# Performance work log

Hardware: AMD Instinct MI355X
Metric: run time of the kernel (lower is better)

The kernel has to match this reference:

```python
import jax, jax.numpy as jnp
import numpy as np

B, M, N = 16384, 512, 2048
N_ITERS = 10


def setup_inputs() -> dict:
    key = jax.random.key(0)
    kb, kD = jax.random.split(key)
    batch = jax.random.normal(kb, (B, M), dtype=jnp.float32)
    # nn.Parameter(torch.rand((M, N))) -> uniform [0,1)
    D = jax.random.uniform(kD, (M, N), dtype=jnp.float32)
    gamma = jnp.float32(0.1)
    beta = jnp.float32(0.1)
    return {"batch": batch, "D": D, "gamma": gamma, "beta": beta}


def reference(batch, D, gamma, beta):
    # Vectorized AMP sparse coding: the original loops over batch items; here
    # the per-sample matvecs D.T@v and D@alpha become batched GEMMs v@D, a@D.T.
    y = batch                                   # [B, M]
    m = D.shape[0]
    sqrt_m = jnp.sqrt(jnp.asarray(m, y.dtype))
    alpha0 = jnp.zeros((y.shape[0], D.shape[1]), dtype=y.dtype)  # [B, N]

    def amp_step(carry, _):
        alpha, v = carry
        z = alpha + beta * (v @ D)                               # [B, N]
        # per-sample threshold t = gamma/sqrt(M) * ||v||_2
        t = (gamma / sqrt_m) * jnp.linalg.norm(v, axis=-1, keepdims=True)  # [B,1]
        new_alpha = jnp.maximum(z - t, 0.0) * jnp.sign(z)        # relu(z-t)*sign(z)
        new_v = (y - beta * (new_alpha @ D.T)
                 + (beta / m) * jnp.linalg.norm(new_alpha, axis=-1, keepdims=True) * v)
        return (new_alpha, new_v), None

    (alpha, _v), _ = jax.lax.scan(amp_step, (alpha0, y), None, length=N_ITERS)
    return alpha
```

## Files before the change

kernel.cpp:

```cpp
#include <hip/hip_runtime.h>
#include <math.h>

#define Bsz 16384
#define Msz 512
#define Nsz 2048

typedef _Float16 half8 __attribute__((ext_vector_type(8)));
typedef _Float16 half4 __attribute__((ext_vector_type(4)));
typedef _Float16 half2v __attribute__((ext_vector_type(2)));
typedef float floatx16 __attribute__((ext_vector_type(16)));
typedef unsigned int uint;

__device__ __forceinline__ void gl_lds16(const _Float16* g, _Float16* l) {
    __builtin_amdgcn_global_load_lds(
        (const __attribute__((address_space(1))) unsigned int*)g,
        (__attribute__((address_space(3))) unsigned int*)l, 16, 0, 0);
}

#define BAR()  asm volatile("s_barrier" ::: "memory")


__global__ __launch_bounds__(256) void zero_kernel(float4* __restrict__ p) {
    p[blockIdx.x * 256 + threadIdx.x] = make_float4(0.f, 0.f, 0.f, 0.f);
}

__global__ __launch_bounds__(256) void init_kernel(const float* __restrict__ batch,
        _Float16* __restrict__ vh, float* __restrict__ t2) {
    const int wave = threadIdx.x >> 6;
    const int lane = threadIdx.x & 63;
    const int b = (blockIdx.x << 2) + wave;
    const float* row = batch + (size_t)b * Msz + lane * 8;
    float4 a = *(const float4*)row;
    float4 c = *(const float4*)(row + 4);
    half8 h;
    h[0] = (_Float16)a.x; h[1] = (_Float16)a.y;
    h[2] = (_Float16)a.z; h[3] = (_Float16)a.w;
    h[4] = (_Float16)c.x; h[5] = (_Float16)c.y;
    h[6] = (_Float16)c.z; h[7] = (_Float16)c.w;
    const size_t off = ((size_t)(b >> 5) * 32 + (lane >> 1)) * 512
                     + ((size_t)(lane & 1) << 8) + ((b & 31) << 3);
    *(half8*)(vh + off) = h;
    float s = a.x*a.x + a.y*a.y + a.z*a.z + a.w*a.w
            + c.x*c.x + c.y*c.y + c.z*c.z + c.w*c.w;
#pragma unroll
    for (int off2 = 32; off2 > 0; off2 >>= 1) s += __shfl_down(s, off2);
    if (lane == 0) t2[b] = s;
}

__global__ __launch_bounds__(256) void convD_kernel(const float* __restrict__ D,
        _Float16* __restrict__ Dph, _Float16* __restrict__ Dtph) {
    __shared__ float T[64][65];
    const int t = threadIdx.x;
    const int tx = t & 15, ty = t >> 4;
    const int n0 = blockIdx.x << 6, m0 = blockIdx.y << 6;
#pragma unroll
    for (int q = 0; q < 4; ++q) {
        const int mr = m0 + (ty << 2) + q;
        const int nc = n0 + (tx << 2);
        float4 d = *(const float4*)(D + (size_t)mr * Nsz + nc);
        half4 h;
        h[0] = (_Float16)d.x; h[1] = (_Float16)d.y;
        h[2] = (_Float16)d.z; h[3] = (_Float16)d.w;
        const size_t o2 = ((size_t)(mr >> 5) * 128 + (nc >> 4)) * 512
                        + (((size_t)(nc >> 3) & 1) << 8) + ((mr & 31) << 3) + (nc & 7);
        *(half4*)(Dph + o2) = h;
        T[(tx << 2) + 0][(ty << 2) + q] = d.x;
        T[(tx << 2) + 1][(ty << 2) + q] = d.y;
        T[(tx << 2) + 2][(ty << 2) + q] = d.z;
        T[(tx << 2) + 3][(ty << 2) + q] = d.w;
    }
    __syncthreads();
#pragma unroll
    for (int q = 0; q < 4; ++q) {
        const int nr = n0 + (ty << 2) + q;
        const int mc = m0 + (tx << 2);
        float4 d = make_float4(T[(ty << 2) + q][tx << 2],
                               T[(ty << 2) + q][(tx << 2) + 1],
                               T[(ty << 2) + q][(tx << 2) + 2],
                               T[(ty << 2) + q][(tx << 2) + 3]);
        half4 h;
        h[0] = (_Float16)d.x; h[1] = (_Float16)d.y;
        h[2] = (_Float16)d.z; h[3] = (_Float16)d.w;
        const size_t o1 = ((size_t)(nr >> 5) * 32 + (mc >> 4)) * 512
                        + (((size_t)(mc >> 3) & 1) << 8) + ((nr & 31) << 3) + (mc & 7);
        *(half4*)(Dtph + o1) = h;
    }
}

template<int FIRST, int LAST>
__global__ __launch_bounds__(256, 4) void gemm1_kernel(
        const _Float16* __restrict__ Av,
        const _Float16* __restrict__ Bth,
        const float* __restrict__ t2,
        _Float16* __restrict__ alphaH,
        float* __restrict__ out,
        float* __restrict__ na2,
        const float* __restrict__ beta_p, const float* __restrict__ gamma_p) {
    const int tid = threadIdx.x;
    const int wave = tid >> 6, lane = tid & 63;
    const int wy = wave >> 1, wx = wave & 1;
    const int ln = lane & 31, lh = lane >> 5;
    const int bid = blockIdx.x;
    const int b0 = (bid & 127) << 7;
    const int n0 = (bid >> 7) << 7;
    const int R0 = b0 >> 5, C0 = n0 >> 5;

    floatx16 acc[2][2] = {};

    const _Float16* pa0 = Av  + ((size_t)(R0 + 2 * wy)     * 32) * 512 + lane * 8;
    const _Float16* pa1 = Av  + ((size_t)(R0 + 2 * wy + 1) * 32) * 512 + lane * 8;
    const _Float16* pb0 = Bth + ((size_t)(C0 + 2 * wx)     * 32) * 512 + lane * 8;
    const _Float16* pb1 = Bth + ((size_t)(C0 + 2 * wx + 1) * 32) * 512 + lane * 8;

    half8 xa0, xa1, xb0, xb1;
    half8 ya0, ya1, yb0, yb1;

    xa0 = *(const half8*)(pa0);
    xa1 = *(const half8*)(pa1);
    xb0 = *(const half8*)(pb0);
    xb1 = *(const half8*)(pb1);

    for (int kt = 0; kt < 32; kt += 2) {
        {
            const size_t o = (size_t)(kt + 1) << 9;
            ya0 = *(const half8*)(pa0 + o);
            ya1 = *(const half8*)(pa1 + o);
            yb0 = *(const half8*)(pb0 + o);
            yb1 = *(const half8*)(pb1 + o);
            acc[0][0] = __builtin_amdgcn_mfma_f32_32x32x16_f16(xa0, xb0, acc[0][0], 0, 0, 0);
            acc[1][0] = __builtin_amdgcn_mfma_f32_32x32x16_f16(xa1, xb0, acc[1][0], 0, 0, 0);
            acc[0][1] = __builtin_amdgcn_mfma_f32_32x32x16_f16(xa0, xb1, acc[0][1], 0, 0, 0);
            acc[1][1] = __builtin_amdgcn_mfma_f32_32x32x16_f16(xa1, xb1, acc[1][1], 0, 0, 0);
        }
        {
            if (kt + 2 < 32) {
                const size_t o = (size_t)(kt + 2) << 9;
                xa0 = *(const half8*)(pa0 + o);
                xa1 = *(const half8*)(pa1 + o);
                xb0 = *(const half8*)(pb0 + o);
                xb1 = *(const half8*)(pb1 + o);
            }
            acc[0][0] = __builtin_amdgcn_mfma_f32_32x32x16_f16(ya0, yb0, acc[0][0], 0, 0, 0);
            acc[1][0] = __builtin_amdgcn_mfma_f32_32x32x16_f16(ya1, yb0, acc[1][0], 0, 0, 0);
            acc[0][1] = __builtin_amdgcn_mfma_f32_32x32x16_f16(ya0, yb1, acc[0][1], 0, 0, 0);
            acc[1][1] = __builtin_amdgcn_mfma_f32_32x32x16_f16(ya1, yb1, acc[1][1], 0, 0, 0);
        }
    }

    const float beta = beta_p[0];
    const float tc = gamma_p[0] * 0.044194173824159216f;
#pragma unroll
    for (int i = 0; i < 2; ++i) {
#pragma unroll
        for (int reg = 0; reg < 16; ++reg) {
            const int rr = (reg & 3) + 8 * (reg >> 2) + 4 * lh;
            const int b = b0 + wy * 64 + i * 32 + rr;
            const float tb2 = tc * sqrtf(t2[b]);
            const size_t rbase = (size_t)b * Nsz + n0 + wx * 64 + ln;
            _Float16* arow = alphaH + rbase;
            float s = 0.f;
#pragma unroll
            for (int j = 0; j < 2; ++j) {
                float z = FIRST ? 0.f : (float)arow[j * 32];
                float val = fmaxf(fmaf(beta, acc[i][j][reg], z) - tb2, 0.f);
                if (LAST) out[rbase + j * 32] = val;
                else      arow[j * 32] = (_Float16)val;
                s = fmaf(val, val, s);
            }
            s += __shfl_down(s, 16, 32);
            s += __shfl_down(s, 8, 32);
            s += __shfl_down(s, 4, 32);
            s += __shfl_down(s, 2, 32);
            s += __shfl_down(s, 1, 32);
            if (ln == 0) atomicAdd(&na2[b], s);
        }
    }
}

__global__ __launch_bounds__(256, 2) void gemm2_kernel(
        const _Float16* __restrict__ alphaH,
        const _Float16* __restrict__ Bh,
        const float* __restrict__ na2,
        const float* __restrict__ y,
        _Float16* __restrict__ vh,
        float* __restrict__ t2,
        const float* __restrict__ beta_p) {
    __shared__ _Float16 lds[16384];

    const int tid = threadIdx.x;
    const int wave = tid >> 6, lane = tid & 63;
    const int wy = wave >> 1, wx = wave & 1;
    const int ln = lane & 31, lh = lane >> 5;
    const int bid = blockIdx.x;
    const int b0 = (bid & 127) << 7;
    const int m0 = (bid >> 7) << 7;
    const int C0 = m0 >> 5;

    floatx16 acc[2][2] = {};

    const int srow = tid >> 1;
    const int skq  = (tid & 1) << 4;
    const _Float16* apP = alphaH + (size_t)(b0 + srow) * Nsz + skq;
    const int awo = ((((srow >> 5) << 1) + (skq >> 4)) << 9) + ((srow & 31) << 3);

    const _Float16* gB = Bh + ((size_t)(C0 + wave) * 128) * 512 + lane * 8;
    const int fB = 8 + wave * 2;

    const int ro = lane << 3;

    uint4 a0, a1;
    auto loadA = [&](int c) {
        const _Float16* nx = apP + c * 32;
        a0 = *(const uint4*)(nx);
        a1 = *(const uint4*)(nx + 8);
    };
    auto writeA = [&](int d) {
        _Float16* aw = lds + d * 8192 + awo;
        *(uint4*)aw = a0;
        *(uint4*)(aw + 256) = a1;
    };
    auto stageB = [&](int c, int d) {
        _Float16* lB = lds + d * 8192;
#pragma unroll
        for (int kt = 0; kt < 2; ++kt)
            gl_lds16(gB + (size_t)kt * 512 + (size_t)c * 1024, lB + ((fB + kt) << 9));
    };

    loadA(0);
    writeA(0);
    stageB(0, 0);
    loadA(1);
    writeA(1);
    stageB(1, 1);
    loadA(2);
    asm volatile("s_waitcnt vmcnt(6) lgkmcnt(0)" ::: "memory");
    BAR();

    for (int c = 0; c < 64; ++c) {
        const _Float16* lb = lds + (c & 1) * 8192;
        __builtin_amdgcn_s_setprio(1);
#pragma unroll
        for (int ks = 0; ks < 2; ++ks) {
            half8 fa[2], fb[2];
#pragma unroll
            for (int i = 0; i < 2; ++i) {
                fa[i] = *(const half8*)(lb + ((((wy * 2 + i) << 1) + ks) << 9) + ro);
                fb[i] = *(const half8*)(lb + 4096 + ((((wx * 2 + i) << 1) + ks) << 9) + ro);
            }
#pragma unroll
            for (int j = 0; j < 2; ++j)
#pragma unroll
                for (int i = 0; i < 2; ++i)
                    acc[i][j] = __builtin_amdgcn_mfma_f32_32x32x16_f16(fa[i], fb[j], acc[i][j], 0, 0, 0);
        }
        __builtin_amdgcn_s_setprio(0);
        if (c == 63) break;
        BAR();
        if (c < 61) {
            stageB(c + 2, c & 1);
            writeA(c & 1);
            loadA(c + 3);
            asm volatile("s_waitcnt vmcnt(6) lgkmcnt(0)" ::: "memory");
        } else if (c == 61) {
            stageB(63, 1);
            writeA(1);
            asm volatile("s_waitcnt vmcnt(2) lgkmcnt(0)" ::: "memory");
        } else {
            asm volatile("s_waitcnt vmcnt(0) lgkmcnt(0)" ::: "memory");
        }
        BAR();
    }

    const float beta = beta_p[0];
#pragma unroll
    for (int i = 0; i < 2; ++i) {
#pragma unroll
        for (int reg = 0; reg < 16; ++reg) {
            const int rr = (reg & 3) + 8 * (reg >> 2) + 4 * lh;
            const int b = b0 + wy * 64 + i * 32 + rr;
            const float cb = beta * (1.0f / 512.0f) * sqrtf(na2[b]);
            float s = 0.f;
#pragma unroll
            for (int j = 0; j < 2; ++j) {
                const int m = m0 + wx * 64 + j * 32 + ln;
                const size_t po = ((size_t)(b >> 5) * 32 + (m >> 4)) * 512
                                + (((size_t)(m >> 3) & 1) << 8) + ((b & 31) << 3) + (m & 7);
                const size_t yi = (size_t)b * Msz + m;
                float vold = (float)vh[po];
                float val = y[yi] - beta * acc[i][j][reg] + cb * vold;
                vh[po] = (_Float16)val;
                s = fmaf(val, val, s);
            }
            s += __shfl_down(s, 16, 32);
            s += __shfl_down(s, 8, 32);
            s += __shfl_down(s, 4, 32);
            s += __shfl_down(s, 2, 32);
            s += __shfl_down(s, 1, 32);
            if (ln == 0) atomicAdd(&t2[b], s);
        }
    }
}

extern "C" void kernel_launch(void* const* d_in, const int* in_sizes, int n_in,
                              void* d_out, int out_size, void* d_ws, size_t ws_size,
                              hipStream_t stream) {
    (void)in_sizes; (void)n_in; (void)out_size; (void)ws_size;
    const float* batch   = (const float*)d_in[0];
    const float* D       = (const float*)d_in[1];
    const float* gamma_p = (const float*)d_in[2];
    const float* beta_p  = (const float*)d_in[3];

    float* out = (float*)d_out;

    _Float16* vh     = (_Float16*)d_ws;
    _Float16* Dph    = vh + (size_t)Bsz * Msz;
    _Float16* Dtph   = Dph + (size_t)Msz * Nsz;
    _Float16* alphaH = Dtph + (size_t)Msz * Nsz;
    float*    t2s    = (float*)(alphaH + (size_t)Bsz * Nsz);
    float*    na2s   = t2s + 10 * Bsz;

    zero_kernel<<<19 * Bsz / 1024, 256, 0, stream>>>((float4*)(t2s + Bsz));
    convD_kernel<<<dim3(Nsz / 64, Msz / 64), 256, 0, stream>>>(D, Dph, Dtph);
    init_kernel<<<Bsz / 4, 256, 0, stream>>>(batch, vh, t2s);

    for (int it = 0; it < 10; ++it) {
        if (it == 0)
            gemm1_kernel<1, 0><<<2048, 256, 0, stream>>>(vh, Dtph,
                    t2s + (size_t)it * Bsz, alphaH, out, na2s + (size_t)it * Bsz,
                    beta_p, gamma_p);
        else if (it == 9)
            gemm1_kernel<0, 1><<<2048, 256, 0, stream>>>(vh, Dtph,
                    t2s + (size_t)it * Bsz, alphaH, out, na2s + (size_t)it * Bsz,
                    beta_p, gamma_p);
        else
            gemm1_kernel<0, 0><<<2048, 256, 0, stream>>>(vh, Dtph,
                    t2s + (size_t)it * Bsz, alphaH, out, na2s + (size_t)it * Bsz,
                    beta_p, gamma_p);
        if (it < 9) {
            gemm2_kernel<<<512, 256, 0, stream>>>(alphaH, Dph,
                                                  na2s + (size_t)it * Bsz,
                                                  batch, vh,
                                                  t2s + (size_t)(it + 1) * Bsz,
                                                  beta_p);
        }
    }
}
```

Before: 1.563 ms.

## Replace LDS-staged gemm2 mainloop with direct global-to-register fragment loads

The gemm2 kernel drops its double-buffered LDS staging (global_load_lds for B, register-to-LDS writes for A, barriers) and has each wave load its MFMA fragments straight from global memory into registers, software-pipelined across two K steps. Launch bounds rise to 4 blocks per CU, which the removed shared memory allows. Separately, the last gemm1 iteration skips the unused alpha-norm reduction and atomics. Without LDS, waves no longer share tiles, so global and L2 traffic grows and loads are less coalesced (rows strided by N), in exchange for no barriers and higher occupancy.

```diff
diff --git a/kernel.cpp b/kernel.cpp
--- a/kernel.cpp
+++ b/kernel.cpp
@@ -7,17 +7,8 @@
 
 typedef _Float16 half8 __attribute__((ext_vector_type(8)));
 typedef _Float16 half4 __attribute__((ext_vector_type(4)));
-typedef _Float16 half2v __attribute__((ext_vector_type(2)));
 typedef float floatx16 __attribute__((ext_vector_type(16)));
 typedef unsigned int uint;
-
-__device__ __forceinline__ void gl_lds16(const _Float16* g, _Float16* l) {
-    __builtin_amdgcn_global_load_lds(
-        (const __attribute__((address_space(1))) unsigned int*)g,
-        (__attribute__((address_space(3))) unsigned int*)l, 16, 0, 0);
-}
-
-#define BAR()  asm volatile("s_barrier" ::: "memory")
 
 
 __global__ __launch_bounds__(256) void zero_kernel(float4* __restrict__ p) {
@@ -167,17 +158,19 @@
                 else      arow[j * 32] = (_Float16)val;
                 s = fmaf(val, val, s);
             }
-            s += __shfl_down(s, 16, 32);
-            s += __shfl_down(s, 8, 32);
-            s += __shfl_down(s, 4, 32);
-            s += __shfl_down(s, 2, 32);
-            s += __shfl_down(s, 1, 32);
-            if (ln == 0) atomicAdd(&na2[b], s);
-        }
-    }
-}
-
-__global__ __launch_bounds__(256, 2) void gemm2_kernel(
+            if (!LAST) {
+                s += __shfl_down(s, 16, 32);
+                s += __shfl_down(s, 8, 32);
+                s += __shfl_down(s, 4, 32);
+                s += __shfl_down(s, 2, 32);
+                s += __shfl_down(s, 1, 32);
+                if (ln == 0) atomicAdd(&na2[b], s);
+            }
+        }
+    }
+}
+
+__global__ __launch_bounds__(256, 4) void gemm2_kernel(
         const _Float16* __restrict__ alphaH,
         const _Float16* __restrict__ Bh,
         const float* __restrict__ na2,
@@ -185,8 +178,6 @@
         _Float16* __restrict__ vh,
         float* __restrict__ t2,
         const float* __restrict__ beta_p) {
-    __shared__ _Float16 lds[16384];
-
     const int tid = threadIdx.x;
     const int wave = tid >> 6, lane = tid & 63;
     const int wy = wave >> 1, wx = wave & 1;
@@ -198,77 +189,46 @@
 
     floatx16 acc[2][2] = {};
 
-    const int srow = tid >> 1;
-    const int skq  = (tid & 1) << 4;
-    const _Float16* apP = alphaH + (size_t)(b0 + srow) * Nsz + skq;
-    const int awo = ((((srow >> 5) << 1) + (skq >> 4)) << 9) + ((srow & 31) << 3);
-
-    const _Float16* gB = Bh + ((size_t)(C0 + wave) * 128) * 512 + lane * 8;
-    const int fB = 8 + wave * 2;
-
-    const int ro = lane << 3;
-
-    uint4 a0, a1;
-    auto loadA = [&](int c) {
-        const _Float16* nx = apP + c * 32;
-        a0 = *(const uint4*)(nx);
-        a1 = *(const uint4*)(nx + 8);
-    };
-    auto writeA = [&](int d) {
-        _Float16* aw = lds + d * 8192 + awo;
-        *(uint4*)aw = a0;
-        *(uint4*)(aw + 256) = a1;
-    };
-    auto stageB = [&](int c, int d) {
-        _Float16* lB = lds + d * 8192;
-#pragma unroll
-        for (int kt = 0; kt < 2; ++kt)
-            gl_lds16(gB + (size_t)kt * 512 + (size_t)c * 1024, lB + ((fB + kt) << 9));
-    };
-
-    loadA(0);
-    writeA(0);
-    stageB(0, 0);
-    loadA(1);
-    writeA(1);
-    stageB(1, 1);
-    loadA(2);
-    asm volatile("s_waitcnt vmcnt(6) lgkmcnt(0)" ::: "memory");
-    BAR();
-
-    for (int c = 0; c < 64; ++c) {
-        const _Float16* lb = lds + (c & 1) * 8192;
-        __builtin_amdgcn_s_setprio(1);
-#pragma unroll
-        for (int ks = 0; ks < 2; ++ks) {
-            half8 fa[2], fb[2];
-#pragma unroll
-            for (int i = 0; i < 2; ++i) {
-                fa[i] = *(const half8*)(lb + ((((wy * 2 + i) << 1) + ks) << 9) + ro);
-                fb[i] = *(const half8*)(lb + 4096 + ((((wx * 2 + i) << 1) + ks) << 9) + ro);
-            }
-#pragma unroll
-            for (int j = 0; j < 2; ++j)
-#pragma unroll
-                for (int i = 0; i < 2; ++i)
-                    acc[i][j] = __builtin_amdgcn_mfma_f32_32x32x16_f16(fa[i], fb[j], acc[i][j], 0, 0, 0);
-        }
-        __builtin_amdgcn_s_setprio(0);
-        if (c == 63) break;
-        BAR();
-        if (c < 61) {
-            stageB(c + 2, c & 1);
-            writeA(c & 1);
-            loadA(c + 3);
-            asm volatile("s_waitcnt vmcnt(6) lgkmcnt(0)" ::: "memory");
-        } else if (c == 61) {
-            stageB(63, 1);
-            writeA(1);
-            asm volatile("s_waitcnt vmcnt(2) lgkmcnt(0)" ::: "memory");
-        } else {
-            asm volatile("s_waitcnt vmcnt(0) lgkmcnt(0)" ::: "memory");
-        }
-        BAR();
+    const _Float16* pa0 = alphaH + (size_t)(b0 + wy * 64 + 0  + ln) * Nsz + lh * 8;
+    const _Float16* pa1 = alphaH + (size_t)(b0 + wy * 64 + 32 + ln) * Nsz + lh * 8;
+    const _Float16* pb0 = Bh + ((size_t)(C0 + 2 * wx)     * 128) * 512 + lane * 8;
+    const _Float16* pb1 = Bh + ((size_t)(C0 + 2 * wx + 1) * 128) * 512 + lane * 8;
+
+    half8 xa0, xa1, xb0, xb1;
+    half8 ya0, ya1, yb0, yb1;
+
+    xa0 = *(const half8*)(pa0);
+    xa1 = *(const half8*)(pa1);
+    xb0 = *(const half8*)(pb0);
+    xb1 = *(const half8*)(pb1);
+
+    for (int kt = 0; kt < 128; kt += 2) {
+        {
+            const size_t oa = (size_t)(kt + 1) * 16;
+            const size_t ob = (size_t)(kt + 1) << 9;
+            ya0 = *(const half8*)(pa0 + oa);
+            ya1 = *(const half8*)(pa1 + oa);
+            yb0 = *(const half8*)(pb0 + ob);
+            yb1 = *(const half8*)(pb1 + ob);
+            acc[0][0] = __builtin_amdgcn_mfma_f32_32x32x16_f16(xa0, xb0, acc[0][0], 0, 0, 0);
+            acc[1][0] = __builtin_amdgcn_mfma_f32_32x32x16_f16(xa1, xb0, acc[1][0], 0, 0, 0);
+            acc[0][1] = __builtin_amdgcn_mfma_f32_32x32x16_f16(xa0, xb1, acc[0][1], 0, 0, 0);
+            acc[1][1] = __builtin_amdgcn_mfma_f32_32x32x16_f16(xa1, xb1, acc[1][1], 0, 0, 0);
+        }
+        {
+            if (kt + 2 < 128) {
+                const size_t oa = (size_t)(kt + 2) * 16;
+                const size_t ob = (size_t)(kt + 2) << 9;
+                xa0 = *(const half8*)(pa0 + oa);
+                xa1 = *(const half8*)(pa1 + oa);
+                xb0 = *(const half8*)(pb0 + ob);
+                xb1 = *(const half8*)(pb1 + ob);
+            }
+            acc[0][0] = __builtin_amdgcn_mfma_f32_32x32x16_f16(ya0, yb0, acc[0][0], 0, 0, 0);
+            acc[1][0] = __builtin_amdgcn_mfma_f32_32x32x16_f16(ya1, yb0, acc[1][0], 0, 0, 0);
+            acc[0][1] = __builtin_amdgcn_mfma_f32_32x32x16_f16(ya0, yb1, acc[0][1], 0, 0, 0);
+            acc[1][1] = __builtin_amdgcn_mfma_f32_32x32x16_f16(ya1, yb1, acc[1][1], 0, 0, 0);
+        }
     }
 
     const float beta = beta_p[0];
```

Result: slower. 1.838 ms (+17.6%).
